# Performance work log

Hardware: AMD Instinct MI355X
Metric: run time of the kernel (lower is better)

## Reference

```python
import jax, jax.numpy as jnp
import numpy as np

D = 1024      # d_model
B = 16        # batch size
L = 1024      # query length
NE = 20000    # global number of entities
NB = 256      # entities per batch element (with -1 padding)
N_PAD = 32    # padded (-1) entity slots per row


def setup_inputs() -> dict:
    key = jax.random.key(0)
    ks = jax.random.split(key, 10)
    s = 1.0 / np.sqrt(D)  # torch nn.Linear default init range
    query = jax.random.normal(ks[0], (B, L, D), jnp.float32)
    ent_emb = jax.random.normal(ks[1], (NE, D), jnp.float32)
    idx = jax.random.randint(ks[2], (B, NB), 0, NE)
    idx = idx.at[:, -N_PAD:].set(-1)  # padding entities -> masked out
    WQ_w = jax.random.uniform(ks[3], (D, D), jnp.float32, -s, s)
    WQ_b = jax.random.uniform(ks[4], (D,), jnp.float32, -s, s)
    WK_w = jax.random.uniform(ks[5], (D, D), jnp.float32, -s, s)
    WK_b = jax.random.uniform(ks[6], (D,), jnp.float32, -s, s)
    WO_w = jax.random.uniform(ks[7], (D, D), jnp.float32, -s, s)
    WO_b = jax.random.uniform(ks[8], (D,), jnp.float32, -s, s)
    ln_g = jnp.ones((D,), jnp.float32)
    ln_b = jnp.zeros((D,), jnp.float32)
    return dict(query=query, ent_emb=ent_emb, ent_idx_in_batch=idx,
                max_entity_number=512,
                WQ_w=WQ_w, WQ_b=WQ_b, WK_w=WK_w, WK_b=WK_b,
                WO_w=WO_w, WO_b=WO_b, ln_g=ln_g, ln_b=ln_b)


def reference(query, ent_emb, ent_idx_in_batch, max_entity_number,
              WQ_w, WQ_b, WK_w, WK_b, WO_w, WO_b, ln_g, ln_b):
    # mask: 1.0 for real entities, 0.0 for -1 padding. (B, NB, 1)
    mask = (ent_idx_in_batch != -1).astype(query.dtype)[:, :, None]
    # gather per-batch entity embeddings (negative index wraps, then masked)
    ent_g = ent_emb[ent_idx_in_batch]                    # (B, NB, D)
    q = query @ WQ_w.T + WQ_b                            # (B, L, D)
    ent = (ent_g @ WK_w.T + WK_b) * mask                 # (B, NB, D)
    # attention scores with additive mask, then softmax
    w = jnp.einsum('byd,bnd->byn', q, ent)               # (B, L, NB)
    w = w - (1.0 - mask[:, :, 0])[:, None, :] * 100000.0
    w = jax.nn.softmax(w, axis=-1)
    # NOTE: original code uses WK (not WV) for values, and scales AFTER softmax
    d_model = query.shape[-1]
    v = jnp.einsum('byn,bnd->byd', w * (float(d_model) ** -0.5), ent)
    v = v @ WO_w.T + WO_b                                # (B, L, D)
    mu = jnp.mean(v, axis=-1, keepdims=True)
    var = jnp.var(v, axis=-1, keepdims=True)             # biased, as torch LN
    v = (v - mu) / jnp.sqrt(var + 1e-5) * ln_g + ln_b
    return v
```

## Files before the change

kernel.cpp:

```cpp
#include <hip/hip_runtime.h>
#include <hip/hip_bf16.h>
#include <cstdint>
#include <cstddef>

typedef _Float16 f16;
typedef _Float16 f16x8 __attribute__((ext_vector_type(8)));
typedef _Float16 f16x4 __attribute__((ext_vector_type(4)));
typedef float    f32x4 __attribute__((ext_vector_type(4)));

#define DM 1024
#define NBE 256

__global__ __launch_bounds__(256) void prep(
    const float* __restrict__ WO_w, f16* __restrict__ WOr,
    const float* __restrict__ WQ_w, const float* __restrict__ WK_w,
    f16* __restrict__ WQt, f16* __restrict__ WKt,
    const float* __restrict__ ent_emb, const int* __restrict__ idx,
    f16* __restrict__ Egh,
    const float* __restrict__ WQ_b, const float* __restrict__ WK_b,
    float* __restrict__ u, float* __restrict__ wobk) {
  __shared__ float ts[64][65];
  __shared__ float sm4[4];
  int blk = blockIdx.x, tid = threadIdx.x;
  if (blk < 1024) {
    int i = (blk * 256 + tid) * 4;
    float4 v = *(const float4*)(WO_w + i);
    f16x4 o; o.x = (f16)v.x; o.y = (f16)v.y; o.z = (f16)v.z; o.w = (f16)v.w;
    *(f16x4*)(WOr + i) = o;
  } else if (blk < 1536) {
    int t = blk - 1024;
    const float* in = (t >> 8) ? WK_w : WQ_w;
    f16* out = (t >> 8) ? WKt : WQt;
    int bi = ((t >> 4) & 15) * 64, bj = (t & 15) * 64;
    int tx = tid & 63, ty = tid >> 6;
#pragma unroll
    for (int k = 0; k < 16; ++k) {
      int r = ty * 16 + k;
      ts[r][tx] = in[(size_t)(bi + r) * DM + bj + tx];
    }
    __syncthreads();
#pragma unroll
    for (int k = 0; k < 16; ++k) {
      int r = ty * 16 + k;
      out[(size_t)(bj + r) * DM + bi + tx] = (f16)ts[tx][r];
    }
  } else if (blk < 5632) {
    int slot = blk - 1536;
    int e = idx[slot];
    int c = tid * 4;
    f16x4 o;
    if (e < 0) {
      o.x = (f16)0.f; o.y = (f16)0.f; o.z = (f16)0.f; o.w = (f16)0.f;
    } else {
      float4 v = *(const float4*)(ent_emb + (size_t)e * DM + c);
      o.x = (f16)v.x; o.y = (f16)v.y; o.z = (f16)v.z; o.w = (f16)v.w;
    }
    *(f16x4*)(Egh + (size_t)slot * DM + c) = o;
  } else if (blk < 5637) {
    int t = blk - 5632;
    if (t < 4) {
      int k = t * 256 + tid;
      float s = 0.f;
      for (int d = 0; d < 1024; ++d) s += WQ_b[d] * WK_w[(size_t)d * 1024 + k];
      u[k] = s;
    } else {
      float s = 0.f;
      for (int i = tid; i < 1024; i += 256) s += WK_b[i] * WQ_b[i];
#pragma unroll
      for (int d = 1; d < 64; d <<= 1) s += __shfl_xor(s, d);
      int w = tid >> 6;
      if ((tid & 63) == 0) sm4[w] = s;
      __syncthreads();
      if (tid == 0) u[1024] = sm4[0] + sm4[1] + sm4[2] + sm4[3];
    }
  } else {
    int w = tid >> 6, lane = tid & 63;
    int r = (blk - 5637) * 4 + w;
    const float* a = WO_w + (size_t)r * 1024;
    float s = 0.f;
#pragma unroll
    for (int i = 0; i < 16; ++i) s += a[lane + i * 64] * WK_b[lane + i * 64];
#pragma unroll
    for (int d = 1; d < 64; d <<= 1) s += __shfl_xor(s, d);
    if (lane == 0) wobk[r] = s;
  }
}

template <int EPI>
__device__ __forceinline__ void gemm_core(
    const f16* __restrict__ A, const f16* __restrict__ B,
    const float* __restrict__ rowbias, const int* __restrict__ colidx,
    f16* __restrict__ C, int N, int K, int m0, int n0,
    f16* __restrict__ smA, f16* __restrict__ smB) {
  int tid = threadIdx.x;
  int lane = tid & 63, w = tid >> 6;
  int wr = w >> 1, wc = w & 1;
  int l15 = lane & 15, lhi = lane >> 4;
  const f16* Ab = A + (size_t)m0 * K;
  const f16* Bb = B + (size_t)n0 * K;

  f32x4 acc[4][4];
  f32x4 z4 = {0.f, 0.f, 0.f, 0.f};
#pragma unroll
  for (int i = 0; i < 4; ++i)
#pragma unroll
    for (int j = 0; j < 4; ++j) acc[i][j] = z4;

  f16x8 ra[4], rb[4];
#pragma unroll
  for (int p = 0; p < 4; ++p) {
    int e = p * 2048 + tid * 8;
    int row = e >> 6, c8 = (e & 63) >> 3;
    ra[p] = *(const f16x8*)(Ab + (size_t)row * K + c8 * 8);
    rb[p] = *(const f16x8*)(Bb + (size_t)row * K + c8 * 8);
  }
#pragma unroll
  for (int p = 0; p < 4; ++p) {
    int e = p * 2048 + tid * 8;
    int row = e >> 6, c8 = (e & 63) >> 3;
    int off = row * 64 + ((c8 ^ (row & 7)) << 3);
    *(f16x8*)(&smA[off]) = ra[p];
    *(f16x8*)(&smB[off]) = rb[p];
  }

  int nk = K >> 6;
  for (int kt = 0; kt < nk; ++kt) {
    int cur = kt & 1;
    bool pre = (kt + 1 < nk);
    __syncthreads();
    if (pre) {
      const f16* An = Ab + (kt + 1) * 64;
      const f16* Bn = Bb + (kt + 1) * 64;
#pragma unroll
      for (int p = 0; p < 4; ++p) {
        int e = p * 2048 + tid * 8;
        int row = e >> 6, c8 = (e & 63) >> 3;
        ra[p] = *(const f16x8*)(An + (size_t)row * K + c8 * 8);
        rb[p] = *(const f16x8*)(Bn + (size_t)row * K + c8 * 8);
      }
    }
    const f16* As = smA + cur * 8192;
    const f16* Bs = smB + cur * 8192;
    __builtin_amdgcn_s_setprio(1);
#pragma unroll
    for (int kk = 0; kk < 2; ++kk) {
      int c8 = kk * 4 + lhi;
      f16x8 af[4], bf[4];
#pragma unroll
      for (int mi = 0; mi < 4; ++mi) {
        int r = wr * 64 + mi * 16 + l15;
        af[mi] = *(const f16x8*)(As + r * 64 + ((c8 ^ (r & 7)) << 3));
      }
#pragma unroll
      for (int ni = 0; ni < 4; ++ni) {
        int r = wc * 64 + ni * 16 + l15;
        bf[ni] = *(const f16x8*)(Bs + r * 64 + ((c8 ^ (r & 7)) << 3));
      }
#pragma unroll
      for (int mi = 0; mi < 4; ++mi)
#pragma unroll
        for (int ni = 0; ni < 4; ++ni)
          acc[mi][ni] = __builtin_amdgcn_mfma_f32_16x16x32_f16(af[mi], bf[ni], acc[mi][ni], 0, 0, 0);
    }
    __builtin_amdgcn_s_setprio(0);
    if (pre) {
#pragma unroll
      for (int p = 0; p < 4; ++p) {
        int e = p * 2048 + tid * 8;
        int row = e >> 6, c8 = (e & 63) >> 3;
        int off = (cur ^ 1) * 8192 + row * 64 + ((c8 ^ (row & 7)) << 3);
        *(f16x8*)(&smA[off]) = ra[p];
        *(f16x8*)(&smB[off]) = rb[p];
      }
    }
  }

#pragma unroll
  for (int mi = 0; mi < 4; ++mi) {
#pragma unroll
    for (int j = 0; j < 4; ++j) {
      int r = m0 + wr * 64 + mi * 16 + lhi * 4 + j;
      float rbv = (EPI == 3) ? rowbias[r] : 0.f;
#pragma unroll
      for (int ni = 0; ni < 4; ++ni) {
        int cN = n0 + wc * 64 + ni * 16 + l15;
        float v = acc[mi][ni][j];
        if (EPI == 3) { v += rbv; if (colidx[cN] < 0) v = 0.f; }
        C[(size_t)r * N + cN] = (f16)v;
      }
    }
  }
}

__global__ __launch_bounds__(256) void gemm_dual(const f16* __restrict__ A0,
                                                 const f16* __restrict__ A1,
                                                 const f16* __restrict__ B,
                                                 f16* __restrict__ C0,
                                                 f16* __restrict__ C1, int N, int K) {
  __shared__ __align__(16) f16 sA[2 * 8192], sB[2 * 8192];
  const f16* A = blockIdx.z ? A1 : A0;
  f16* C = blockIdx.z ? C1 : C0;
  gemm_core<0>(A, B, nullptr, nullptr, C, N, K, blockIdx.y * 128, blockIdx.x * 128, sA, sB);
}

__global__ __launch_bounds__(256) void gemm_pair(
    const f16* __restrict__ Egh, const f16* __restrict__ G, const f16* __restrict__ H,
    const float* __restrict__ wobk, const int* __restrict__ idx,
    const float* __restrict__ u,
    f16* __restrict__ Tp, f16* __restrict__ EWot, float* __restrict__ cvec) {
  __shared__ __align__(16) f16 sA[2 * 8192], sB[2 * 8192];
  int blk = blockIdx.x;
  if (blk < 256) {
    gemm_core<0>(Egh, G, nullptr, nullptr, Tp, 1024, 1024, (blk >> 3) * 128, (blk & 7) * 128, sA, sB);
  } else if (blk < 512) {
    int t = blk - 256;
    gemm_core<3>(H, Egh, wobk, idx, EWot, 4096, 1024, (t >> 5) * 128, (t & 31) * 128, sA, sB);
  } else {
    int t = blk - 512;
    int w = threadIdx.x >> 6, lane = threadIdx.x & 63;
    int n = t * 4 + w;
    const f16* e = Egh + (size_t)n * 1024;
    float s = 0.f;
#pragma unroll
    for (int i = 0; i < 16; ++i) { int k = lane + i * 64; s += (float)e[k] * u[k]; }
#pragma unroll
    for (int d = 1; d < 64; d <<= 1) s += __shfl_xor(s, d);
    if (lane == 0)
      cvec[n] = s + u[1024] + ((idx[n] < 0) ? -100000.0f : 0.0f);
  }
}

__global__ __launch_bounds__(256, 2) void attn3(
    const float* __restrict__ query, const f16* __restrict__ Tp,
    const f16* __restrict__ EWot, const float* __restrict__ cvec,
    f16* __restrict__ O16) {
  __shared__ __align__(16) char pool[49152];
  f16* smB = (f16*)pool;
  f16* smP = (f16*)(pool + 32768);
  f16* smQ = (f16*)(pool + 32768);
  __shared__ float smMax[64], smSum[64];
  int id = blockIdx.x;
  int b = id & 15, lt = id >> 4;
  int tid = threadIdx.x, lane = tid & 63, w = tid >> 6;
  int l15 = lane & 15, lhi = lane >> 4;
  int wq = w >> 1, wc = w & 1;
  const float* Qb = query + (size_t)(b * 1024 + lt * 32) * DM;
  const f16* Tb = Tp + (size_t)b * NBE * DM;

  f32x4 z4 = {0.f, 0.f, 0.f, 0.f};
  f32x4 accs[8];
#pragma unroll
  for (int i = 0; i < 8; ++i) accs[i] = z4;

  float4 rqa, rqb;
  f16x8 rb[8];
  int qrow = tid >> 3, qc0 = (tid & 7) * 8;

  rqa = *(const float4*)(Qb + (size_t)qrow * DM + qc0);
  rqb = *(const float4*)(Qb + (size_t)qrow * DM + qc0 + 4);
#pragma unroll
  for (int p = 0; p < 8; ++p) {
    int e = p * 2048 + tid * 8;
    int row = e >> 6, c8 = (e & 63) >> 3;
    rb[p] = *(const f16x8*)(Tb + (size_t)row * DM + c8 * 8);
  }

  for (int kt = 0; kt < 16; ++kt) {
    __syncthreads();
    {
      f16x8 h;
      h[0] = (f16)rqa.x; h[1] = (f16)rqa.y; h[2] = (f16)rqa.z; h[3] = (f16)rqa.w;
      h[4] = (f16)rqb.x; h[5] = (f16)rqb.y; h[6] = (f16)rqb.z; h[7] = (f16)rqb.w;
      int c8 = qc0 >> 3;
      *(f16x8*)(smQ + qrow * 64 + ((c8 ^ (qrow & 7)) << 3)) = h;
    }
#pragma unroll
    for (int p = 0; p < 8; ++p) {
      int e = p * 2048 + tid * 8;
      int row = e >> 6, c8 = (e & 63) >> 3;
      *(f16x8*)(smB + row * 64 + ((c8 ^ (row & 7)) << 3)) = rb[p];
    }
    __syncthreads();
    if (kt < 15) {
      rqa = *(const float4*)(Qb + (size_t)qrow * DM + (kt + 1) * 64 + qc0);
      rqb = *(const float4*)(Qb + (size_t)qrow * DM + (kt + 1) * 64 + qc0 + 4);
#pragma unroll
      for (int p = 0; p < 8; ++p) {
        int e = p * 2048 + tid * 8;
        int row = e >> 6, c8 = (e & 63) >> 3;
        rb[p] = *(const f16x8*)(Tb + (size_t)row * DM + (kt + 1) * 64 + c8 * 8);
      }
    }
    __builtin_amdgcn_s_setprio(1);
#pragma unroll
    for (int kk = 0; kk < 2; ++kk) {
      int c8 = kk * 4 + lhi;
      int qr = wq * 16 + l15;
      f16x8 aq = *(const f16x8*)(smQ + qr * 64 + ((c8 ^ (qr & 7)) << 3));
#pragma unroll
      for (int ni = 0; ni < 8; ++ni) {
        int er = wc * 128 + ni * 16 + l15;
        f16x8 bb = *(const f16x8*)(smB + er * 64 + ((c8 ^ (er & 7)) << 3));
        accs[ni] = __builtin_amdgcn_mfma_f32_16x16x32_f16(aq, bb, accs[ni], 0, 0, 0);
      }
    }
    __builtin_amdgcn_s_setprio(0);
  }

  const f16* Eb = EWot + (size_t)b * NBE;
#pragma unroll
  for (int p = 0; p < 8; ++p) {
    int e = p * 2048 + tid * 8;
    int row = e >> 6, c8 = (e & 63) >> 3;
    rb[p] = *(const f16x8*)(Eb + (size_t)row * 4096 + c8 * 8);
  }

  float cv[8];
#pragma unroll
  for (int ni = 0; ni < 8; ++ni)
    cv[ni] = cvec[b * NBE + wc * 128 + ni * 16 + l15];
  int rbase = wq * 16 + lhi * 4;
  float mxl[4], sml[4];
#pragma unroll
  for (int j = 0; j < 4; ++j) {
    float m = -3.0e38f;
#pragma unroll
    for (int ni = 0; ni < 8; ++ni) m = fmaxf(m, accs[ni][j] + cv[ni]);
    m = fmaxf(m, __shfl_xor(m, 1));
    m = fmaxf(m, __shfl_xor(m, 2));
    m = fmaxf(m, __shfl_xor(m, 4));
    m = fmaxf(m, __shfl_xor(m, 8));
    mxl[j] = m;
    if (l15 == 0) smMax[wc * 32 + rbase + j] = m;
  }
  __syncthreads();
#pragma unroll
  for (int j = 0; j < 4; ++j) {
    float fm = fmaxf(mxl[j], smMax[(wc ^ 1) * 32 + rbase + j]);
    float s = 0.f;
#pragma unroll
    for (int ni = 0; ni < 8; ++ni) {
      float e = __expf(accs[ni][j] + cv[ni] - fm);
      accs[ni][j] = e;
      s += e;
    }
    s += __shfl_xor(s, 1);
    s += __shfl_xor(s, 2);
    s += __shfl_xor(s, 4);
    s += __shfl_xor(s, 8);
    sml[j] = s;
    if (l15 == 0) smSum[wc * 32 + rbase + j] = s;
  }
  __syncthreads();
#pragma unroll
  for (int j = 0; j < 4; ++j) {
    float inv = 0.03125f / (sml[j] + smSum[(wc ^ 1) * 32 + rbase + j]);
    int r = rbase + j;
#pragma unroll
    for (int ni = 0; ni < 8; ++ni) {
      int col = wc * 128 + ni * 16 + l15;
      int cc8 = col >> 3;
      smP[r * 256 + ((cc8 ^ (r & 7)) << 3) + (col & 7)] = (f16)(accs[ni][j] * inv);
    }
  }

  f16* Ob = O16 + (size_t)(b * 1024 + lt * 32) * DM;
  for (int dc = 0; dc < 4; ++dc) {
    f32x4 accv[8];
#pragma unroll
    for (int i = 0; i < 8; ++i) accv[i] = z4;
    for (int ks = 0; ks < 4; ++ks) {
      __syncthreads();
#pragma unroll
      for (int p = 0; p < 8; ++p) {
        int e = p * 2048 + tid * 8;
        int row = e >> 6, c8 = (e & 63) >> 3;
        *(f16x8*)(smB + row * 64 + ((c8 ^ (row & 7)) << 3)) = rb[p];
      }
      __syncthreads();
      int nxt = dc * 4 + ks + 1;
      if (nxt < 16) {
        int ndc = nxt >> 2, nks = nxt & 3;
#pragma unroll
        for (int p = 0; p < 8; ++p) {
          int e = p * 2048 + tid * 8;
          int row = e >> 6, c8 = (e & 63) >> 3;
          rb[p] = *(const f16x8*)(Eb + (size_t)(ndc * 256 + row) * 4096 + nks * 64 + c8 * 8);
        }
      }
      __builtin_amdgcn_s_setprio(1);
#pragma unroll
      for (int kk = 0; kk < 2; ++kk) {
        int pc8 = ks * 8 + kk * 4 + lhi;
        int qr = wq * 16 + l15;
        f16x8 ap = *(const f16x8*)(smP + qr * 256 + ((pc8 ^ (qr & 7)) << 3));
        int c8 = kk * 4 + lhi;
#pragma unroll
        for (int ni = 0; ni < 8; ++ni) {
          int er = wc * 128 + ni * 16 + l15;
          f16x8 bv = *(const f16x8*)(smB + er * 64 + ((c8 ^ (er & 7)) << 3));
          accv[ni] = __builtin_amdgcn_mfma_f32_16x16x32_f16(ap, bv, accv[ni], 0, 0, 0);
        }
      }
      __builtin_amdgcn_s_setprio(0);
    }
#pragma unroll
    for (int ni = 0; ni < 8; ++ni) {
#pragma unroll
      for (int j = 0; j < 4; ++j) {
        int r = wq * 16 + lhi * 4 + j;
        int col = dc * 256 + wc * 128 + ni * 16 + l15;
        Ob[(size_t)r * DM + col] = (f16)accv[ni][j];
      }
    }
  }
}

__global__ __launch_bounds__(256) void ln_f16(const f16* __restrict__ X,
                                              const float* __restrict__ bo,
                                              const float* __restrict__ g,
                                              const float* __restrict__ bta,
                                              float* __restrict__ out) {
  size_t row = blockIdx.x;
  const f16* x = X + row * DM;
  int tid = threadIdx.x;
  f16x4 h = *(const f16x4*)(x + tid * 4);
  float4 bo4 = *(const float4*)(bo + tid * 4);
  float4 v;
  v.x = (float)h[0] + bo4.x; v.y = (float)h[1] + bo4.y;
  v.z = (float)h[2] + bo4.z; v.w = (float)h[3] + bo4.w;
  float s = v.x + v.y + v.z + v.w;
  float q = v.x * v.x + v.y * v.y + v.z * v.z + v.w * v.w;
#pragma unroll
  for (int d = 1; d < 64; d <<= 1) { s += __shfl_xor(s, d); q += __shfl_xor(q, d); }
  __shared__ float ss[4], qq[4];
  int w = tid >> 6, lane = tid & 63;
  if (lane == 0) { ss[w] = s; qq[w] = q; }
  __syncthreads();
  s = ss[0] + ss[1] + ss[2] + ss[3];
  q = qq[0] + qq[1] + qq[2] + qq[3];
  float mu = s * (1.0f / DM);
  float var = q * (1.0f / DM) - mu * mu;
  float rs = rsqrtf(var + 1e-5f);
  float4 gg = *(const float4*)(g + tid * 4);
  float4 bb = *(const float4*)(bta + tid * 4);
  float4 o;
  o.x = (v.x - mu) * rs * gg.x + bb.x;
  o.y = (v.y - mu) * rs * gg.y + bb.y;
  o.z = (v.z - mu) * rs * gg.z + bb.z;
  o.w = (v.w - mu) * rs * gg.w + bb.w;
  *(float4*)(out + row * DM + tid * 4) = o;
}

extern "C" void kernel_launch(void* const* d_in, const int* in_sizes, int n_in,
                              void* d_out, int out_size, void* d_ws, size_t ws_size,
                              hipStream_t stream) {
  const float* query   = (const float*)d_in[0];
  const float* ent_emb = (const float*)d_in[1];
  const int*   idx     = (const int*)d_in[2];
  const float* WQ_w = (const float*)d_in[4];
  const float* WQ_b = (const float*)d_in[5];
  const float* WK_w = (const float*)d_in[6];
  const float* WK_b = (const float*)d_in[7];
  const float* WO_w = (const float*)d_in[8];
  const float* WO_b = (const float*)d_in[9];
  const float* ln_g = (const float*)d_in[10];
  const float* ln_b = (const float*)d_in[11];
  float* out = (float*)d_out;

  char* p = (char*)d_ws;
  f16* Egh  = (f16*)p;  p += (size_t)4096 * 1024 * 2;
  f16* WQt  = (f16*)p;  p += (size_t)1024 * 1024 * 2;
  f16* WKt  = (f16*)p;  p += (size_t)1024 * 1024 * 2;
  f16* WOr  = (f16*)p;  p += (size_t)1024 * 1024 * 2;
  f16* G    = (f16*)p;  p += (size_t)1024 * 1024 * 2;
  f16* H    = (f16*)p;  p += (size_t)1024 * 1024 * 2;
  f16* Tp   = (f16*)p;  p += (size_t)4096 * 1024 * 2;
  f16* EWot = (f16*)p;  p += (size_t)1024 * 4096 * 2;
  f16* O16  = (f16*)p;  p += (size_t)16384 * 1024 * 2;
  float* u    = (float*)p; p += 1025 * 4;
  float* wobk = (float*)p; p += 1024 * 4;
  float* cvec = (float*)p; p += 4096 * 4;

  prep<<<5893, 256, 0, stream>>>(WO_w, WOr, WQ_w, WK_w, WQt, WKt,
                                 ent_emb, idx, Egh, WQ_b, WK_b, u, wobk);
  gemm_dual<<<dim3(8, 8, 2), 256, 0, stream>>>(WQt, WOr, WKt, G, H, 1024, 1024);
  gemm_pair<<<1536, 256, 0, stream>>>(Egh, G, H, wobk, idx, u, Tp, EWot, cvec);
  attn3<<<512, 256, 0, stream>>>(query, Tp, EWot, cvec, O16);
  ln_f16<<<16384, 256, 0, stream>>>(O16, WO_b, ln_g, ln_b, out);
}
```

Measured before the change: 308.0 us.

## Reassociate weight products, rewrite attention without LDS staging, wave-per-row layernorm

Instead of precomputing the weight-by-weight products WQ·WK and WO·WK, the entities are first projected through WK (an entity GEMM of size 4096×1024×1024), and that result is then multiplied by WQ and WO. This drops the 1024³ weight-weight GEMMs and the u-vector loop. The attention kernel now uses 512 threads with 8 waves that read Q and T operands straight from global memory into MFMA registers, with no LDS staging. The waves split the entity dimension four ways and combine softmax statistics through shared memory. Layernorm now handles one row per wave with no block sync, and the large-entity GEMM costs more FLOPs than the old weight GEMMs.

```diff
diff --git a/kernel.cpp b/kernel.cpp
--- a/kernel.cpp
+++ b/kernel.cpp
@@ -12,41 +12,18 @@
 #define NBE 256
 
 __global__ __launch_bounds__(256) void prep(
-    const float* __restrict__ WO_w, f16* __restrict__ WOr,
-    const float* __restrict__ WQ_w, const float* __restrict__ WK_w,
-    f16* __restrict__ WQt, f16* __restrict__ WKt,
     const float* __restrict__ ent_emb, const int* __restrict__ idx,
     f16* __restrict__ Egh,
+    const float* __restrict__ WK_w, f16* __restrict__ WKr,
+    const float* __restrict__ WO_w, f16* __restrict__ WOr,
+    const float* __restrict__ WQ_w, f16* __restrict__ WQt,
     const float* __restrict__ WQ_b, const float* __restrict__ WK_b,
-    float* __restrict__ u, float* __restrict__ wobk) {
+    float* __restrict__ wobk, float* __restrict__ bqbk) {
   __shared__ float ts[64][65];
   __shared__ float sm4[4];
   int blk = blockIdx.x, tid = threadIdx.x;
-  if (blk < 1024) {
-    int i = (blk * 256 + tid) * 4;
-    float4 v = *(const float4*)(WO_w + i);
-    f16x4 o; o.x = (f16)v.x; o.y = (f16)v.y; o.z = (f16)v.z; o.w = (f16)v.w;
-    *(f16x4*)(WOr + i) = o;
-  } else if (blk < 1536) {
-    int t = blk - 1024;
-    const float* in = (t >> 8) ? WK_w : WQ_w;
-    f16* out = (t >> 8) ? WKt : WQt;
-    int bi = ((t >> 4) & 15) * 64, bj = (t & 15) * 64;
-    int tx = tid & 63, ty = tid >> 6;
-#pragma unroll
-    for (int k = 0; k < 16; ++k) {
-      int r = ty * 16 + k;
-      ts[r][tx] = in[(size_t)(bi + r) * DM + bj + tx];
-    }
-    __syncthreads();
-#pragma unroll
-    for (int k = 0; k < 16; ++k) {
-      int r = ty * 16 + k;
-      out[(size_t)(bj + r) * DM + bi + tx] = (f16)ts[tx][r];
-    }
-  } else if (blk < 5632) {
-    int slot = blk - 1536;
-    int e = idx[slot];
+  if (blk < 4096) {
+    int e = idx[blk];
     int c = tid * 4;
     f16x4 o;
     if (e < 0) {
@@ -55,27 +32,41 @@
       float4 v = *(const float4*)(ent_emb + (size_t)e * DM + c);
       o.x = (f16)v.x; o.y = (f16)v.y; o.z = (f16)v.z; o.w = (f16)v.w;
     }
-    *(f16x4*)(Egh + (size_t)slot * DM + c) = o;
-  } else if (blk < 5637) {
-    int t = blk - 5632;
-    if (t < 4) {
-      int k = t * 256 + tid;
-      float s = 0.f;
-      for (int d = 0; d < 1024; ++d) s += WQ_b[d] * WK_w[(size_t)d * 1024 + k];
-      u[k] = s;
-    } else {
-      float s = 0.f;
-      for (int i = tid; i < 1024; i += 256) s += WK_b[i] * WQ_b[i];
-#pragma unroll
-      for (int d = 1; d < 64; d <<= 1) s += __shfl_xor(s, d);
-      int w = tid >> 6;
-      if ((tid & 63) == 0) sm4[w] = s;
-      __syncthreads();
-      if (tid == 0) u[1024] = sm4[0] + sm4[1] + sm4[2] + sm4[3];
-    }
-  } else {
+    *(f16x4*)(Egh + (size_t)blk * DM + c) = o;
+  } else if (blk < 4608) {
+    int i = (blk - 4096) * 2048 + tid * 8;
+    float4 a = *(const float4*)(WK_w + i);
+    float4 b = *(const float4*)(WK_w + i + 4);
+    f16x8 o;
+    o[0] = (f16)a.x; o[1] = (f16)a.y; o[2] = (f16)a.z; o[3] = (f16)a.w;
+    o[4] = (f16)b.x; o[5] = (f16)b.y; o[6] = (f16)b.z; o[7] = (f16)b.w;
+    *(f16x8*)(WKr + i) = o;
+  } else if (blk < 5120) {
+    int i = (blk - 4608) * 2048 + tid * 8;
+    float4 a = *(const float4*)(WO_w + i);
+    float4 b = *(const float4*)(WO_w + i + 4);
+    f16x8 o;
+    o[0] = (f16)a.x; o[1] = (f16)a.y; o[2] = (f16)a.z; o[3] = (f16)a.w;
+    o[4] = (f16)b.x; o[5] = (f16)b.y; o[6] = (f16)b.z; o[7] = (f16)b.w;
+    *(f16x8*)(WOr + i) = o;
+  } else if (blk < 5376) {
+    int t = blk - 5120;
+    int bi = ((t >> 4) & 15) * 64, bj = (t & 15) * 64;
+    int tx = tid & 63, ty = tid >> 6;
+#pragma unroll
+    for (int k = 0; k < 16; ++k) {
+      int r = ty * 16 + k;
+      ts[r][tx] = WQ_w[(size_t)(bi + r) * DM + bj + tx];
+    }
+    __syncthreads();
+#pragma unroll
+    for (int k = 0; k < 16; ++k) {
+      int r = ty * 16 + k;
+      WQt[(size_t)(bj + r) * DM + bi + tx] = (f16)ts[tx][r];
+    }
+  } else if (blk < 5632) {
     int w = tid >> 6, lane = tid & 63;
-    int r = (blk - 5637) * 4 + w;
+    int r = (blk - 5376) * 4 + w;
     const float* a = WO_w + (size_t)r * 1024;
     float s = 0.f;
 #pragma unroll
@@ -83,6 +74,15 @@
 #pragma unroll
     for (int d = 1; d < 64; d <<= 1) s += __shfl_xor(s, d);
     if (lane == 0) wobk[r] = s;
+  } else {
+    float s = 0.f;
+    for (int i = tid; i < 1024; i += 256) s += WK_b[i] * WQ_b[i];
+#pragma unroll
+    for (int d = 1; d < 64; d <<= 1) s += __shfl_xor(s, d);
+    int w = tid >> 6;
+    if ((tid & 63) == 0) sm4[w] = s;
+    __syncthreads();
+    if (tid == 0) bqbk[0] = sm4[0] + sm4[1] + sm4[2] + sm4[3];
   }
 }
 
@@ -192,264 +192,194 @@
   }
 }
 
-__global__ __launch_bounds__(256) void gemm_dual(const f16* __restrict__ A0,
-                                                 const f16* __restrict__ A1,
-                                                 const f16* __restrict__ B,
-                                                 f16* __restrict__ C0,
-                                                 f16* __restrict__ C1, int N, int K) {
+__global__ __launch_bounds__(256) void gemm_e0(const f16* __restrict__ Egh,
+                                               const f16* __restrict__ WKr,
+                                               f16* __restrict__ E0) {
   __shared__ __align__(16) f16 sA[2 * 8192], sB[2 * 8192];
-  const f16* A = blockIdx.z ? A1 : A0;
-  f16* C = blockIdx.z ? C1 : C0;
-  gemm_core<0>(A, B, nullptr, nullptr, C, N, K, blockIdx.y * 128, blockIdx.x * 128, sA, sB);
-}
-
-__global__ __launch_bounds__(256) void gemm_pair(
-    const f16* __restrict__ Egh, const f16* __restrict__ G, const f16* __restrict__ H,
-    const float* __restrict__ wobk, const int* __restrict__ idx,
-    const float* __restrict__ u,
+  gemm_core<0>(Egh, WKr, nullptr, nullptr, E0, 1024, 1024,
+               blockIdx.y * 128, blockIdx.x * 128, sA, sB);
+}
+
+__global__ __launch_bounds__(256) void stage3(
+    const f16* __restrict__ E0, const f16* __restrict__ WQt,
+    const f16* __restrict__ WOr, const float* __restrict__ wobk,
+    const int* __restrict__ idx, const float* __restrict__ bq,
+    const float* __restrict__ bqbk,
     f16* __restrict__ Tp, f16* __restrict__ EWot, float* __restrict__ cvec) {
   __shared__ __align__(16) f16 sA[2 * 8192], sB[2 * 8192];
   int blk = blockIdx.x;
   if (blk < 256) {
-    gemm_core<0>(Egh, G, nullptr, nullptr, Tp, 1024, 1024, (blk >> 3) * 128, (blk & 7) * 128, sA, sB);
+    gemm_core<0>(E0, WQt, nullptr, nullptr, Tp, 1024, 1024,
+                 (blk >> 3) * 128, (blk & 7) * 128, sA, sB);
   } else if (blk < 512) {
     int t = blk - 256;
-    gemm_core<3>(H, Egh, wobk, idx, EWot, 4096, 1024, (t >> 5) * 128, (t & 31) * 128, sA, sB);
+    gemm_core<3>(WOr, E0, wobk, idx, EWot, 4096, 1024,
+                 (t >> 5) * 128, (t & 31) * 128, sA, sB);
   } else {
     int t = blk - 512;
     int w = threadIdx.x >> 6, lane = threadIdx.x & 63;
     int n = t * 4 + w;
-    const f16* e = Egh + (size_t)n * 1024;
+    const f16* e = E0 + (size_t)n * 1024;
     float s = 0.f;
 #pragma unroll
-    for (int i = 0; i < 16; ++i) { int k = lane + i * 64; s += (float)e[k] * u[k]; }
+    for (int i = 0; i < 16; ++i) { int k = lane + i * 64; s += (float)e[k] * bq[k]; }
 #pragma unroll
     for (int d = 1; d < 64; d <<= 1) s += __shfl_xor(s, d);
     if (lane == 0)
-      cvec[n] = s + u[1024] + ((idx[n] < 0) ? -100000.0f : 0.0f);
-  }
-}
-
-__global__ __launch_bounds__(256, 2) void attn3(
+      cvec[n] = s + bqbk[0] + ((idx[n] < 0) ? -100000.0f : 0.0f);
+  }
+}
+
+__global__ __launch_bounds__(512, 4) void attn5(
     const float* __restrict__ query, const f16* __restrict__ Tp,
     const f16* __restrict__ EWot, const float* __restrict__ cvec,
     f16* __restrict__ O16) {
-  __shared__ __align__(16) char pool[49152];
-  f16* smB = (f16*)pool;
-  f16* smP = (f16*)(pool + 32768);
-  f16* smQ = (f16*)(pool + 32768);
-  __shared__ float smMax[64], smSum[64];
+  __shared__ __align__(16) f16 smP[32 * 256];
+  __shared__ float smMax[4][32], smSum[4][32];
   int id = blockIdx.x;
   int b = id & 15, lt = id >> 4;
   int tid = threadIdx.x, lane = tid & 63, w = tid >> 6;
   int l15 = lane & 15, lhi = lane >> 4;
-  int wq = w >> 1, wc = w & 1;
-  const float* Qb = query + (size_t)(b * 1024 + lt * 32) * DM;
-  const f16* Tb = Tp + (size_t)b * NBE * DM;
+  int wm = w >> 2, we = w & 3;
+  const float* Qb = query + (size_t)(b * 1024 + lt * 32 + wm * 16) * DM;
+  const f16* Tb = Tp + (size_t)(b * NBE + we * 64) * DM;
 
   f32x4 z4 = {0.f, 0.f, 0.f, 0.f};
-  f32x4 accs[8];
-#pragma unroll
-  for (int i = 0; i < 8; ++i) accs[i] = z4;
-
-  float4 rqa, rqb;
-  f16x8 rb[8];
-  int qrow = tid >> 3, qc0 = (tid & 7) * 8;
-
-  rqa = *(const float4*)(Qb + (size_t)qrow * DM + qc0);
-  rqb = *(const float4*)(Qb + (size_t)qrow * DM + qc0 + 4);
-#pragma unroll
-  for (int p = 0; p < 8; ++p) {
-    int e = p * 2048 + tid * 8;
-    int row = e >> 6, c8 = (e & 63) >> 3;
-    rb[p] = *(const f16x8*)(Tb + (size_t)row * DM + c8 * 8);
-  }
-
+  f32x4 acc[4];
+#pragma unroll
+  for (int i = 0; i < 4; ++i) acc[i] = z4;
+
+  const float* qrow = Qb + (size_t)l15 * DM + lhi * 8;
   for (int kt = 0; kt < 16; ++kt) {
-    __syncthreads();
-    {
+    int k0 = kt * 64;
+    f16x8 bb[4][2];
+#pragma unroll
+    for (int ni = 0; ni < 4; ++ni)
+#pragma unroll
+      for (int kk = 0; kk < 2; ++kk)
+        bb[ni][kk] = *(const f16x8*)(Tb + (size_t)(ni * 16 + l15) * DM + k0 + kk * 32 + lhi * 8);
+    f16x8 aq[2];
+#pragma unroll
+    for (int kk = 0; kk < 2; ++kk) {
+      float4 qa = *(const float4*)(qrow + k0 + kk * 32);
+      float4 qc = *(const float4*)(qrow + k0 + kk * 32 + 4);
       f16x8 h;
-      h[0] = (f16)rqa.x; h[1] = (f16)rqa.y; h[2] = (f16)rqa.z; h[3] = (f16)rqa.w;
-      h[4] = (f16)rqb.x; h[5] = (f16)rqb.y; h[6] = (f16)rqb.z; h[7] = (f16)rqb.w;
-      int c8 = qc0 >> 3;
-      *(f16x8*)(smQ + qrow * 64 + ((c8 ^ (qrow & 7)) << 3)) = h;
-    }
-#pragma unroll
-    for (int p = 0; p < 8; ++p) {
-      int e = p * 2048 + tid * 8;
-      int row = e >> 6, c8 = (e & 63) >> 3;
-      *(f16x8*)(smB + row * 64 + ((c8 ^ (row & 7)) << 3)) = rb[p];
-    }
-    __syncthreads();
-    if (kt < 15) {
-      rqa = *(const float4*)(Qb + (size_t)qrow * DM + (kt + 1) * 64 + qc0);
-      rqb = *(const float4*)(Qb + (size_t)qrow * DM + (kt + 1) * 64 + qc0 + 4);
-#pragma unroll
-      for (int p = 0; p < 8; ++p) {
-        int e = p * 2048 + tid * 8;
-        int row = e >> 6, c8 = (e & 63) >> 3;
-        rb[p] = *(const f16x8*)(Tb + (size_t)row * DM + (kt + 1) * 64 + c8 * 8);
-      }
-    }
-    __builtin_amdgcn_s_setprio(1);
-#pragma unroll
-    for (int kk = 0; kk < 2; ++kk) {
-      int c8 = kk * 4 + lhi;
-      int qr = wq * 16 + l15;
-      f16x8 aq = *(const f16x8*)(smQ + qr * 64 + ((c8 ^ (qr & 7)) << 3));
-#pragma unroll
-      for (int ni = 0; ni < 8; ++ni) {
-        int er = wc * 128 + ni * 16 + l15;
-        f16x8 bb = *(const f16x8*)(smB + er * 64 + ((c8 ^ (er & 7)) << 3));
-        accs[ni] = __builtin_amdgcn_mfma_f32_16x16x32_f16(aq, bb, accs[ni], 0, 0, 0);
-      }
-    }
-    __builtin_amdgcn_s_setprio(0);
-  }
-
-  const f16* Eb = EWot + (size_t)b * NBE;
-#pragma unroll
-  for (int p = 0; p < 8; ++p) {
-    int e = p * 2048 + tid * 8;
-    int row = e >> 6, c8 = (e & 63) >> 3;
-    rb[p] = *(const f16x8*)(Eb + (size_t)row * 4096 + c8 * 8);
-  }
-
-  float cv[8];
-#pragma unroll
-  for (int ni = 0; ni < 8; ++ni)
-    cv[ni] = cvec[b * NBE + wc * 128 + ni * 16 + l15];
-  int rbase = wq * 16 + lhi * 4;
-  float mxl[4], sml[4];
+      h[0] = (f16)qa.x; h[1] = (f16)qa.y; h[2] = (f16)qa.z; h[3] = (f16)qa.w;
+      h[4] = (f16)qc.x; h[5] = (f16)qc.y; h[6] = (f16)qc.z; h[7] = (f16)qc.w;
+      aq[kk] = h;
+    }
+#pragma unroll
+    for (int kk = 0; kk < 2; ++kk)
+#pragma unroll
+      for (int ni = 0; ni < 4; ++ni)
+        acc[ni] = __builtin_amdgcn_mfma_f32_16x16x32_f16(aq[kk], bb[ni][kk], acc[ni], 0, 0, 0);
+  }
+
+  float cv[4];
+#pragma unroll
+  for (int ni = 0; ni < 4; ++ni)
+    cv[ni] = cvec[b * NBE + we * 64 + ni * 16 + l15];
+  int rbase = wm * 16 + lhi * 4;
 #pragma unroll
   for (int j = 0; j < 4; ++j) {
     float m = -3.0e38f;
 #pragma unroll
-    for (int ni = 0; ni < 8; ++ni) m = fmaxf(m, accs[ni][j] + cv[ni]);
+    for (int ni = 0; ni < 4; ++ni) m = fmaxf(m, acc[ni][j] + cv[ni]);
     m = fmaxf(m, __shfl_xor(m, 1));
     m = fmaxf(m, __shfl_xor(m, 2));
     m = fmaxf(m, __shfl_xor(m, 4));
     m = fmaxf(m, __shfl_xor(m, 8));
-    mxl[j] = m;
-    if (l15 == 0) smMax[wc * 32 + rbase + j] = m;
+    if (l15 == 0) smMax[we][rbase + j] = m;
   }
   __syncthreads();
 #pragma unroll
   for (int j = 0; j < 4; ++j) {
-    float fm = fmaxf(mxl[j], smMax[(wc ^ 1) * 32 + rbase + j]);
+    int r = rbase + j;
+    float fm = fmaxf(fmaxf(smMax[0][r], smMax[1][r]), fmaxf(smMax[2][r], smMax[3][r]));
     float s = 0.f;
 #pragma unroll
-    for (int ni = 0; ni < 8; ++ni) {
-      float e = __expf(accs[ni][j] + cv[ni] - fm);
-      accs[ni][j] = e;
+    for (int ni = 0; ni < 4; ++ni) {
+      float e = __expf(acc[ni][j] + cv[ni] - fm);
+      acc[ni][j] = e;
       s += e;
     }
     s += __shfl_xor(s, 1);
     s += __shfl_xor(s, 2);
     s += __shfl_xor(s, 4);
     s += __shfl_xor(s, 8);
-    sml[j] = s;
-    if (l15 == 0) smSum[wc * 32 + rbase + j] = s;
+    if (l15 == 0) smSum[we][r] = s;
   }
   __syncthreads();
 #pragma unroll
   for (int j = 0; j < 4; ++j) {
-    float inv = 0.03125f / (sml[j] + smSum[(wc ^ 1) * 32 + rbase + j]);
     int r = rbase + j;
-#pragma unroll
-    for (int ni = 0; ni < 8; ++ni) {
-      int col = wc * 128 + ni * 16 + l15;
-      int cc8 = col >> 3;
-      smP[r * 256 + ((cc8 ^ (r & 7)) << 3) + (col & 7)] = (f16)(accs[ni][j] * inv);
-    }
-  }
-
-  f16* Ob = O16 + (size_t)(b * 1024 + lt * 32) * DM;
+    float inv = 0.03125f / (smSum[0][r] + smSum[1][r] + smSum[2][r] + smSum[3][r]);
+#pragma unroll
+    for (int ni = 0; ni < 4; ++ni) {
+      int col = we * 64 + ni * 16 + l15;
+      smP[r * 256 + (((col >> 3) ^ (r & 7)) << 3) + (col & 7)] = (f16)(acc[ni][j] * inv);
+    }
+  }
+  __syncthreads();
+
+  f16x8 pa[8];
+  {
+    int pr = wm * 16 + l15;
+#pragma unroll
+    for (int ks = 0; ks < 8; ++ks)
+      pa[ks] = *(const f16x8*)(smP + pr * 256 + (((ks * 4 + lhi) ^ (pr & 7)) << 3));
+  }
+  const f16* Eb = EWot + b * NBE + lhi * 8;
+  f16* Ob = O16 + (size_t)(b * 1024 + lt * 32 + wm * 16) * DM;
   for (int dc = 0; dc < 4; ++dc) {
-    f32x4 accv[8];
-#pragma unroll
-    for (int i = 0; i < 8; ++i) accv[i] = z4;
-    for (int ks = 0; ks < 4; ++ks) {
-      __syncthreads();
-#pragma unroll
-      for (int p = 0; p < 8; ++p) {
-        int e = p * 2048 + tid * 8;
-        int row = e >> 6, c8 = (e & 63) >> 3;
-        *(f16x8*)(smB + row * 64 + ((c8 ^ (row & 7)) << 3)) = rb[p];
-      }
-      __syncthreads();
-      int nxt = dc * 4 + ks + 1;
-      if (nxt < 16) {
-        int ndc = nxt >> 2, nks = nxt & 3;
-#pragma unroll
-        for (int p = 0; p < 8; ++p) {
-          int e = p * 2048 + tid * 8;
-          int row = e >> 6, c8 = (e & 63) >> 3;
-          rb[p] = *(const f16x8*)(Eb + (size_t)(ndc * 256 + row) * 4096 + nks * 64 + c8 * 8);
-        }
-      }
-      __builtin_amdgcn_s_setprio(1);
-#pragma unroll
-      for (int kk = 0; kk < 2; ++kk) {
-        int pc8 = ks * 8 + kk * 4 + lhi;
-        int qr = wq * 16 + l15;
-        f16x8 ap = *(const f16x8*)(smP + qr * 256 + ((pc8 ^ (qr & 7)) << 3));
-        int c8 = kk * 4 + lhi;
-#pragma unroll
-        for (int ni = 0; ni < 8; ++ni) {
-          int er = wc * 128 + ni * 16 + l15;
-          f16x8 bv = *(const f16x8*)(smB + er * 64 + ((c8 ^ (er & 7)) << 3));
-          accv[ni] = __builtin_amdgcn_mfma_f32_16x16x32_f16(ap, bv, accv[ni], 0, 0, 0);
-        }
-      }
-      __builtin_amdgcn_s_setprio(0);
-    }
-#pragma unroll
-    for (int ni = 0; ni < 8; ++ni) {
-#pragma unroll
-      for (int j = 0; j < 4; ++j) {
-        int r = wq * 16 + lhi * 4 + j;
-        int col = dc * 256 + wc * 128 + ni * 16 + l15;
-        Ob[(size_t)r * DM + col] = (f16)accv[ni][j];
-      }
-    }
-  }
-}
-
-__global__ __launch_bounds__(256) void ln_f16(const f16* __restrict__ X,
-                                              const float* __restrict__ bo,
-                                              const float* __restrict__ g,
-                                              const float* __restrict__ bta,
-                                              float* __restrict__ out) {
-  size_t row = blockIdx.x;
-  const f16* x = X + row * DM;
-  int tid = threadIdx.x;
-  f16x4 h = *(const f16x4*)(x + tid * 4);
-  float4 bo4 = *(const float4*)(bo + tid * 4);
-  float4 v;
-  v.x = (float)h[0] + bo4.x; v.y = (float)h[1] + bo4.y;
-  v.z = (float)h[2] + bo4.z; v.w = (float)h[3] + bo4.w;
-  float s = v.x + v.y + v.z + v.w;
-  float q = v.x * v.x + v.y * v.y + v.z * v.z + v.w * v.w;
+    f32x4 accv[4];
+#pragma unroll
+    for (int i = 0; i < 4; ++i) accv[i] = z4;
+#pragma unroll
+    for (int ks = 0; ks < 8; ++ks) {
+      f16x8 bv[4];
+#pragma unroll
+      for (int ni = 0; ni < 4; ++ni)
+        bv[ni] = *(const f16x8*)(Eb + (size_t)(we * 256 + dc * 64 + ni * 16 + l15) * 4096 + ks * 32);
+#pragma unroll
+      for (int ni = 0; ni < 4; ++ni)
+        accv[ni] = __builtin_amdgcn_mfma_f32_16x16x32_f16(pa[ks], bv[ni], accv[ni], 0, 0, 0);
+    }
+#pragma unroll
+    for (int ni = 0; ni < 4; ++ni)
+#pragma unroll
+      for (int j = 0; j < 4; ++j)
+        Ob[(size_t)(lhi * 4 + j) * DM + we * 256 + dc * 64 + ni * 16 + l15] = (f16)accv[ni][j];
+  }
+}
+
+__global__ __launch_bounds__(256) void ln5(const f16* __restrict__ X,
+                                           const float* __restrict__ bo,
+                                           const float* __restrict__ g,
+                                           const float* __restrict__ bta,
+                                           float* __restrict__ out) {
+  int lane = threadIdx.x & 63;
+  size_t row = blockIdx.x * 4 + (threadIdx.x >> 6);
+  const f16* x = X + row * DM + lane * 16;
+  f16x8 h0 = *(const f16x8*)(x);
+  f16x8 h1 = *(const f16x8*)(x + 8);
+  float v[16];
+#pragma unroll
+  for (int i = 0; i < 8; ++i) { v[i] = (float)h0[i]; v[8 + i] = (float)h1[i]; }
+#pragma unroll
+  for (int i = 0; i < 16; ++i) v[i] += bo[lane * 16 + i];
+  float s = 0.f, q = 0.f;
+#pragma unroll
+  for (int i = 0; i < 16; ++i) { s += v[i]; q += v[i] * v[i]; }
 #pragma unroll
   for (int d = 1; d < 64; d <<= 1) { s += __shfl_xor(s, d); q += __shfl_xor(q, d); }
-  __shared__ float ss[4], qq[4];
-  int w = tid >> 6, lane = tid & 63;
-  if (lane == 0) { ss[w] = s; qq[w] = q; }
-  __syncthreads();
-  s = ss[0] + ss[1] + ss[2] + ss[3];
-  q = qq[0] + qq[1] + qq[2] + qq[3];
   float mu = s * (1.0f / DM);
   float var = q * (1.0f / DM) - mu * mu;
   float rs = rsqrtf(var + 1e-5f);
-  float4 gg = *(const float4*)(g + tid * 4);
-  float4 bb = *(const float4*)(bta + tid * 4);
-  float4 o;
-  o.x = (v.x - mu) * rs * gg.x + bb.x;
-  o.y = (v.y - mu) * rs * gg.y + bb.y;
-  o.z = (v.z - mu) * rs * gg.z + bb.z;
-  o.w = (v.w - mu) * rs * gg.w + bb.w;
-  *(float4*)(out + row * DM + tid * 4) = o;
+  float* o = out + row * DM + lane * 16;
+#pragma unroll
+  for (int i = 0; i < 16; ++i)
+    o[i] = (v[i] - mu) * rs * g[lane * 16 + i] + bta[lane * 16 + i];
 }
 
 extern "C" void kernel_launch(void* const* d_in, const int* in_sizes, int n_in,
@@ -470,22 +400,22 @@
 
   char* p = (char*)d_ws;
   f16* Egh  = (f16*)p;  p += (size_t)4096 * 1024 * 2;
+  f16* WKr  = (f16*)p;  p += (size_t)1024 * 1024 * 2;
+  f16* WOr  = (f16*)p;  p += (size_t)1024 * 1024 * 2;
   f16* WQt  = (f16*)p;  p += (size_t)1024 * 1024 * 2;
-  f16* WKt  = (f16*)p;  p += (size_t)1024 * 1024 * 2;
-  f16* WOr  = (f16*)p;  p += (size_t)1024 * 1024 * 2;
-  f16* G    = (f16*)p;  p += (size_t)1024 * 1024 * 2;
-  f16* H    = (f16*)p;  p += (size_t)1024 * 1024 * 2;
+  f16* E0   = (f16*)p;  p += (size_t)4096 * 1024 * 2;
   f16* Tp   = (f16*)p;  p += (size_t)4096 * 1024 * 2;
   f16* EWot = (f16*)p;  p += (size_t)1024 * 4096 * 2;
   f16* O16  = (f16*)p;  p += (size_t)16384 * 1024 * 2;
-  float* u    = (float*)p; p += 1025 * 4;
   float* wobk = (float*)p; p += 1024 * 4;
+  float* bqbk = (float*)p; p += 4;
   float* cvec = (float*)p; p += 4096 * 4;
 
-  prep<<<5893, 256, 0, stream>>>(WO_w, WOr, WQ_w, WK_w, WQt, WKt,
-                                 ent_emb, idx, Egh, WQ_b, WK_b, u, wobk);
-  gemm_dual<<<dim3(8, 8, 2), 256, 0, stream>>>(WQt, WOr, WKt, G, H, 1024, 1024);
-  gemm_pair<<<1536, 256, 0, stream>>>(Egh, G, H, wobk, idx, u, Tp, EWot, cvec);
-  attn3<<<512, 256, 0, stream>>>(query, Tp, EWot, cvec, O16);
-  ln_f16<<<16384, 256, 0, stream>>>(O16, WO_b, ln_g, ln_b, out);
-}
+  prep<<<5633, 256, 0, stream>>>(ent_emb, idx, Egh, WK_w, WKr, WO_w, WOr,
+                                 WQ_w, WQt, WQ_b, WK_b, wobk, bqbk);
+  gemm_e0<<<dim3(8, 32), 256, 0, stream>>>(Egh, WKr, E0);
+  stage3<<<1536, 256, 0, stream>>>(E0, WQt, WOr, wobk, idx, WQ_b, bqbk,
+                                   Tp, EWot, cvec);
+  attn5<<<512, 512, 0, stream>>>(query, Tp, EWot, cvec, O16);
+  ln5<<<4096, 256, 0, stream>>>(O16, WO_b, ln_g, ln_b, out);
+}
```

Result: slower. 393.9 us (+27.9%).
